# Performance work log

Hardware: AMD Instinct MI355X
Metric: run time of the kernel (lower is better)

The kernel has to match this reference:

```python
import jax, jax.numpy as jnp
import numpy as np
import math

DIM = 1024
D_FF = 1024
B = 128


def setup_inputs() -> dict:
    key = jax.random.key(0)
    ks = jax.random.split(key, 13)
    s = 1.0 / math.sqrt(DIM)
    sf = 1.0 / math.sqrt(D_FF)
    return {
        "x": jax.random.normal(ks[0], (B, DIM), dtype=jnp.float32),
        "Wq": jax.random.uniform(ks[1], (DIM, DIM), jnp.float32, -s, s),
        "bq": jax.random.uniform(ks[2], (DIM,), jnp.float32, -s, s),
        "Wk": jax.random.uniform(ks[3], (DIM, DIM), jnp.float32, -s, s),
        "bk": jax.random.uniform(ks[4], (DIM,), jnp.float32, -s, s),
        "Wv": jax.random.uniform(ks[5], (DIM, DIM), jnp.float32, -s, s),
        "bv": jax.random.uniform(ks[6], (DIM,), jnp.float32, -s, s),
        "Wo": jax.random.uniform(ks[7], (DIM, DIM), jnp.float32, -s, s),
        "bo": jax.random.uniform(ks[8], (DIM,), jnp.float32, -s, s),
        "W1": jax.random.uniform(ks[9], (D_FF, DIM), jnp.float32, -s, s),
        "b1": jax.random.uniform(ks[10], (D_FF,), jnp.float32, -s, s),
        "W2": jax.random.uniform(ks[11], (DIM, D_FF), jnp.float32, -sf, sf),
        "b2": jax.random.uniform(ks[12], (DIM,), jnp.float32, -sf, sf),
    }


def reference(x, Wq, bq, Wk, bk, Wv, bv, Wo, bo, W1, b1, W2, b2):
    # Attention (eval mode: dropout is identity)
    q = x @ Wq.T + bq                      # [B, D]
    k = x @ Wk.T + bk                      # [B, D]
    v = x @ Wv.T + bv                      # [B, D]
    inv_sqrt_dk = 1.0 / math.sqrt(DIM)
    # per-sample outer product: weights[b, i, j] = q[b,i] * k[b,j] / sqrt(d_k)
    weights = (q[:, :, None] * k[:, None, :]) * inv_sqrt_dk  # [B, D, D]
    nw = jax.nn.softmax(weights, axis=-1)                    # [B, D, D]
    attn_out = jnp.einsum('bij,bj->bi', nw, v)               # [B, D]
    attn_out = attn_out @ Wo.T + bo
    # residual 1
    x2 = x + attn_out
    # FFN
    h = jax.nn.relu(x2 @ W1.T + b1)        # [B, d_ff]
    ff = h @ W2.T + b2                     # [B, D]
    out = x2 + ff
    return (out, nw)
```

## Files before the change

kernel.cpp:

```cpp
#include <hip/hip_runtime.h>

#define DIM   1024
#define BATCH 128
#define MAT   (BATCH*DIM)
#define NROWS MAT
#define DS    32

typedef float f4n __attribute__((ext_vector_type(4)));

#define Q_AT  28672
#define A_WO  28672
#define B_WO  47104
#define A_W1  54272
#define B_W1  72704
#define A_W2  79872
#define B_W2  98304
#define MBASE 105472

struct Params {
  const float *x,*Wq,*bq,*Wk,*bk,*Wv,*bv,*Wo,*bo,*W1,*b1,*W2,*b2;
  float *out,*nw;
  float *q,*k,*v,*araw,*x2,*h,*P;
};

template<bool WRITE, bool AR>
__device__ __forceinline__ void attn_range(const Params& p, int r0, int r1, int lane)
{
  int bcur = -1;
  float4 kr[4], vr[4];
#pragma unroll 1
  for (int row = r0; row < r1; ++row) {
    const int b = row >> 10;
    if (b != bcur) {
      bcur = b;
      const float4* __restrict__ k4 = (const float4*)(p.k + ((size_t)b<<10));
#pragma unroll
      for (int t=0;t<4;++t) kr[t] = k4[lane + 64*t];
      if (AR) {
        const float4* __restrict__ v4 = (const float4*)(p.v + ((size_t)b<<10));
#pragma unroll
        for (int t=0;t<4;++t) vr[t] = v4[lane + 64*t];
      }
    }
    const float c = p.q[row] * 0.03125f;
    float sum=0.f, dot=0.f;
    float4 e[4];
#pragma unroll
    for (int t=0;t<4;++t) {
      const float4 kk = kr[t];
      float4 pp;
      pp.x=__expf(c*kk.x); pp.y=__expf(c*kk.y);
      pp.z=__expf(c*kk.z); pp.w=__expf(c*kk.w);
      sum += (pp.x+pp.y)+(pp.z+pp.w);
      if (AR) {
        const float4 vv = vr[t];
        dot += pp.x*vv.x + pp.y*vv.y + pp.z*vv.z + pp.w*vv.w;
      }
      e[t]=pp;
    }
#pragma unroll
    for (int off=32; off>=1; off>>=1) {
      sum += __shfl_xor(sum, off);
      if (AR) dot += __shfl_xor(dot, off);
    }
    const float rinv = 1.f/sum;
    if (WRITE) {
      f4n* o = (f4n*)(p.nw + ((size_t)row<<10));
#pragma unroll
      for (int t=0;t<4;++t) {
        const float4 pp=e[t];
        f4n st;
        st.x = pp.x*rinv; st.y = pp.y*rinv;
        st.z = pp.z*rinv; st.w = pp.w*rinv;
        __builtin_nontemporal_store(st, &o[lane + 64*t]);
      }
    }
    if (AR && lane==0) p.araw[row] = dot*rinv;
  }
}

__device__ __forceinline__ void gemm_tile(
    const float* __restrict__ X, const float* __restrict__ W,
    float* __restrict__ Pout, int n0, int k0, int KC,
    float* xt, float* wt)
{
  const int tid = threadIdx.x;
  const int tn = tid & 15, tb = tid >> 4;
  const int b_base = tb*8, n_base = tn*4;
  float acc[8][4];
#pragma unroll
  for (int i=0;i<8;++i)
#pragma unroll
    for (int j=0;j<4;++j) acc[i][j]=0.f;

  for (int s=0; s<KC/DS; ++s) {
    const int kk = k0 + s*DS;
#pragma unroll
    for (int r=0;r<4;++r) {
      const int row = (tid>>3) + 32*r;
      const int c0  = (tid&7)*4;
      const float4 vv = *(const float4*)(X + (size_t)row*DIM + kk + c0);
      xt[(c0+0)*132+row]=vv.x; xt[(c0+1)*132+row]=vv.y;
      xt[(c0+2)*132+row]=vv.z; xt[(c0+3)*132+row]=vv.w;
    }
#pragma unroll
    for (int r=0;r<2;++r) {
      const int row = (tid>>3) + 32*r;
      const int c0  = (tid&7)*4;
      const f4n vv = __builtin_nontemporal_load(
          (const f4n*)(W + (size_t)(n0+row)*DIM + kk + c0));
      wt[(c0+0)*68+row]=vv.x; wt[(c0+1)*68+row]=vv.y;
      wt[(c0+2)*68+row]=vv.z; wt[(c0+3)*68+row]=vv.w;
    }
    __syncthreads();
#pragma unroll 4
    for (int d=0; d<DS; ++d) {
      const float4 xa0 = *(const float4*)&xt[d*132 + b_base];
      const float4 xa1 = *(const float4*)&xt[d*132 + b_base + 4];
      const float4 wa  = *(const float4*)&wt[d*68  + n_base];
      const float xr[8] = {xa0.x,xa0.y,xa0.z,xa0.w, xa1.x,xa1.y,xa1.z,xa1.w};
      const float wr[4] = {wa.x,wa.y,wa.z,wa.w};
#pragma unroll
      for (int bb=0;bb<8;++bb)
#pragma unroll
        for (int nn=0;nn<4;++nn) acc[bb][nn] += xr[bb]*wr[nn];
    }
    __syncthreads();
  }
#pragma unroll
  for (int bb=0;bb<8;++bb) {
    const float4 st = make_float4(acc[bb][0],acc[bb][1],acc[bb][2],acc[bb][3]);
    *(float4*)(Pout + (size_t)(b_base+bb)*DIM + n0 + n_base) = st;
  }
}

__global__ __launch_bounds__(256) void qkv_partial(
    const float* __restrict__ X, const float* __restrict__ W0,
    const float* __restrict__ W1, const float* __restrict__ W2,
    float* __restrict__ P)
{
  __shared__ float xt[DS*132];
  __shared__ float wt[DS*68];
  const int z = blockIdx.z;
  const float* W = (z==0)?W0:(z==1)?W1:W2;
  gemm_tile(X, W, P + (size_t)(z*8+blockIdx.y)*MAT,
            blockIdx.x*64, blockIdx.y*128, 128, xt, wt);
}

__global__ __launch_bounds__(256) void qkv_reduce(Params p)
{
  const int t = blockIdx.x*256 + threadIdx.x;
  const int z = t >> 15, idx4 = t & 32767;
  const float4* Pz = (const float4*)(p.P + (size_t)z*8*MAT);
  const float*  bias = (z==0) ? p.bq : (z==1) ? p.bk : p.bv;
  float* outz = (z==0) ? p.q : (z==1) ? p.k : p.v;
  float4 s = Pz[idx4];
#pragma unroll
  for (int sp=1; sp<8; ++sp) {
    const float4 t2 = Pz[sp*(MAT/4)+idx4];
    s.x+=t2.x; s.y+=t2.y; s.z+=t2.z; s.w+=t2.w;
  }
  const float4 b4 = ((const float4*)bias)[idx4 & 255];
  s.x+=b4.x; s.y+=b4.y; s.z+=b4.z; s.w+=b4.w;
  ((float4*)outz)[idx4] = s;
}

__global__ __launch_bounds__(256,4) void attn_mixed(Params p)
{
  const int bid = blockIdx.x, tid = threadIdx.x;
  const int wave = tid>>6, lane = tid&63;
  if (bid < 768) {
    const int gw = bid*4 + wave;
    int r0 = gw*43, r1 = r0 + 43;
    if (r1 > NROWS) r1 = NROWS;
    attn_range<false,true>(p, r0, r1, lane);
  } else {
    const int gw2 = (bid-768)*4 + wave;
    attn_range<true,false>(p, gw2*28, gw2*28 + 28, lane);
  }
}

__global__ __launch_bounds__(256,4) void chainA(Params p,
    const float* __restrict__ X, const float* __restrict__ W, int wbase)
{
  __shared__ float xt[DS*132];
  __shared__ float wt[DS*68];
  const int bid = blockIdx.x, tid = threadIdx.x;
  const int wave = tid>>6, lane = tid&63;
  if (bid < 256) {
    gemm_tile(X, W, p.P + (size_t)(bid&15)*MAT, (bid>>4)*64, (bid&15)*64, 64, xt, wt);
  } else {
    const int gw = (bid-256)*4 + wave;
    attn_range<true,false>(p, wbase + gw*6, wbase + gw*6 + 6, lane);
  }
}

__global__ __launch_bounds__(256,4) void chainB(Params p,
    const float* __restrict__ bias, const float* __restrict__ extra,
    float* __restrict__ out, int relu, int wbase)
{
  const int bid = blockIdx.x, tid = threadIdx.x;
  const int wave = tid>>6, lane = tid&63;
  if (bid < 128) {
    const int idx4 = bid*256 + tid;
    const float4* P4 = (const float4*)p.P;
    float4 s = P4[idx4];
#pragma unroll
    for (int sp=1; sp<16; ++sp) {
      const float4 t2 = P4[sp*(MAT/4)+idx4];
      s.x+=t2.x; s.y+=t2.y; s.z+=t2.z; s.w+=t2.w;
    }
    const float4 b4 = ((const float4*)bias)[idx4 & 255];
    s.x+=b4.x; s.y+=b4.y; s.z+=b4.z; s.w+=b4.w;
    if (relu) { s.x=fmaxf(s.x,0.f); s.y=fmaxf(s.y,0.f);
                s.z=fmaxf(s.z,0.f); s.w=fmaxf(s.w,0.f); }
    if (extra) {
      const float4 e = ((const float4*)extra)[idx4];
      s.x+=e.x; s.y+=e.y; s.z+=e.z; s.w+=e.w;
    }
    ((float4*)out)[idx4] = s;
  } else {
    const int gw = (bid-128)*4 + wave;
    attn_range<true,false>(p, wbase + gw*2, wbase + gw*2 + 2, lane);
  }
}

__global__ __launch_bounds__(256,4) void mopup(Params p)
{
  const int gw = blockIdx.x*4 + (threadIdx.x>>6);
  const int lane = threadIdx.x & 63;
  int r0, n;
  if (gw < 1024) { r0 = MBASE + gw*7;             n = 7; }
  else           { r0 = MBASE + 7168 + (gw-1024)*6; n = 6; }
  attn_range<true,false>(p, r0, r0 + n, lane);
}

extern "C" void kernel_launch(void* const* d_in, const int* in_sizes, int n_in,
                              void* d_out, int out_size, void* d_ws, size_t ws_size,
                              hipStream_t stream)
{
  (void)in_sizes; (void)n_in; (void)out_size; (void)ws_size;
  Params p;
  p.x  = (const float*)d_in[0];
  p.Wq = (const float*)d_in[1];  p.bq = (const float*)d_in[2];
  p.Wk = (const float*)d_in[3];  p.bk = (const float*)d_in[4];
  p.Wv = (const float*)d_in[5];  p.bv = (const float*)d_in[6];
  p.Wo = (const float*)d_in[7];  p.bo = (const float*)d_in[8];
  p.W1 = (const float*)d_in[9];  p.b1 = (const float*)d_in[10];
  p.W2 = (const float*)d_in[11]; p.b2 = (const float*)d_in[12];
  p.out = (float*)d_out;
  p.nw  = p.out + MAT;
  float* ws = (float*)d_ws;
  p.q    = ws;         p.k  = ws + MAT;   p.v = ws + 2*MAT;
  p.araw = ws + 3*MAT; p.x2 = ws + 4*MAT; p.h = ws + 5*MAT;
  p.P    = ws + 6*MAT;

  qkv_partial<<<dim3(16,8,3), 256, 0, stream>>>(p.x, p.Wq, p.Wk, p.Wv, p.P);
  qkv_reduce<<<384, 256, 0, stream>>>(p);

  attn_mixed<<<1024, 256, 0, stream>>>(p);

  chainA<<<1024, 256, 0, stream>>>(p, p.araw, p.Wo, A_WO);
  chainB<<<1024, 256, 0, stream>>>(p, p.bo, p.x, p.x2, 0, B_WO);

  chainA<<<1024, 256, 0, stream>>>(p, p.x2, p.W1, A_W1);
  chainB<<<1024, 256, 0, stream>>>(p, p.b1, nullptr, p.h, 1, B_W1);

  chainA<<<1024, 256, 0, stream>>>(p, p.h, p.W2, A_W2);
  chainB<<<1024, 256, 0, stream>>>(p, p.b2, p.x2, p.out, 0, B_W2);

  mopup<<<1024, 256, 0, stream>>>(p);
}
```

Baseline: 177.7 us.

## Cache softmax reciprocal sums and deepen split-K in chained GEMM stages

The first attention pass, which already computes each row's softmax sum for the attention output, now also saves the reciprocal sum to a workspace buffer. Every later pass that writes normalized weights reuses it, so those passes do only exp, scale and store, with no cross-lane sum reduction. The chained Wo/W1/W2 GEMMs move from 16-way to 32-way split-K with 512 GEMM blocks. The row ranges given to each overlapped stage are rebalanced to match. In exchange the workspace needs room for one more buffer plus twice as many partial-sum slabs, and each reduce step reads 32 partials instead of 16.

```diff
diff --git a/kernel.cpp b/kernel.cpp
--- a/kernel.cpp
+++ b/kernel.cpp
@@ -10,21 +10,21 @@
 
 #define Q_AT  28672
 #define A_WO  28672
-#define B_WO  47104
-#define A_W1  54272
-#define B_W1  72704
-#define A_W2  79872
-#define B_W2  98304
-#define MBASE 105472
+#define B_WO  43008
+#define A_W1  50176
+#define B_W1  64512
+#define A_W2  71680
+#define B_W2  86016
+#define MBASE 93184
 
 struct Params {
   const float *x,*Wq,*bq,*Wk,*bk,*Wv,*bv,*Wo,*bo,*W1,*b1,*W2,*b2;
   float *out,*nw;
-  float *q,*k,*v,*araw,*x2,*h,*P;
+  float *q,*k,*v,*araw,*x2,*h,*rinv,*P;
 };
 
-template<bool WRITE, bool AR>
-__device__ __forceinline__ void attn_range(const Params& p, int r0, int r1, int lane)
+template<bool WRITE, bool AR, bool USE_RINV>
+__device__ __forceinline__ void attn_rows(const Params& p, int r0, int r1, int lane)
 {
   int bcur = -1;
   float4 kr[4], vr[4];
@@ -43,6 +43,21 @@
       }
     }
     const float c = p.q[row] * 0.03125f;
+
+    if (WRITE && USE_RINV) {
+      const float rinv = p.rinv[row];
+      f4n* o = (f4n*)(p.nw + ((size_t)row<<10));
+#pragma unroll
+      for (int t=0;t<4;++t) {
+        const float4 kk = kr[t];
+        f4n st;
+        st.x = __expf(c*kk.x)*rinv; st.y = __expf(c*kk.y)*rinv;
+        st.z = __expf(c*kk.z)*rinv; st.w = __expf(c*kk.w)*rinv;
+        __builtin_nontemporal_store(st, &o[lane + 64*t]);
+      }
+      continue;
+    }
+
     float sum=0.f, dot=0.f;
     float4 e[4];
 #pragma unroll
@@ -75,7 +90,7 @@
         __builtin_nontemporal_store(st, &o[lane + 64*t]);
       }
     }
-    if (AR && lane==0) p.araw[row] = dot*rinv;
+    if (AR && lane==0) { p.araw[row] = dot*rinv; p.rinv[row] = rinv; }
   }
 }
 
@@ -173,10 +188,10 @@
     const int gw = bid*4 + wave;
     int r0 = gw*43, r1 = r0 + 43;
     if (r1 > NROWS) r1 = NROWS;
-    attn_range<false,true>(p, r0, r1, lane);
+    attn_rows<false,true,false>(p, r0, r1, lane);
   } else {
     const int gw2 = (bid-768)*4 + wave;
-    attn_range<true,false>(p, gw2*28, gw2*28 + 28, lane);
+    attn_rows<true,false,false>(p, gw2*28, gw2*28 + 28, lane);
   }
 }
 
@@ -187,11 +202,12 @@
   __shared__ float wt[DS*68];
   const int bid = blockIdx.x, tid = threadIdx.x;
   const int wave = tid>>6, lane = tid&63;
-  if (bid < 256) {
-    gemm_tile(X, W, p.P + (size_t)(bid&15)*MAT, (bid>>4)*64, (bid&15)*64, 64, xt, wt);
+  if (bid < 512) {
+    const int nt = bid >> 5, sp = bid & 31;
+    gemm_tile(X, W, p.P + (size_t)sp*MAT, nt*64, sp*32, 32, xt, wt);
   } else {
-    const int gw = (bid-256)*4 + wave;
-    attn_range<true,false>(p, wbase + gw*6, wbase + gw*6 + 6, lane);
+    const int gw = (bid-512)*4 + wave;
+    attn_rows<true,false,true>(p, wbase + gw*7, wbase + gw*7 + 7, lane);
   }
 }
 
@@ -206,7 +222,7 @@
     const float4* P4 = (const float4*)p.P;
     float4 s = P4[idx4];
 #pragma unroll
-    for (int sp=1; sp<16; ++sp) {
+    for (int sp=1; sp<32; ++sp) {
       const float4 t2 = P4[sp*(MAT/4)+idx4];
       s.x+=t2.x; s.y+=t2.y; s.z+=t2.z; s.w+=t2.w;
     }
@@ -221,7 +237,7 @@
     ((float4*)out)[idx4] = s;
   } else {
     const int gw = (bid-128)*4 + wave;
-    attn_range<true,false>(p, wbase + gw*2, wbase + gw*2 + 2, lane);
+    attn_rows<true,false,true>(p, wbase + gw*2, wbase + gw*2 + 2, lane);
   }
 }
 
@@ -230,9 +246,9 @@
   const int gw = blockIdx.x*4 + (threadIdx.x>>6);
   const int lane = threadIdx.x & 63;
   int r0, n;
-  if (gw < 1024) { r0 = MBASE + gw*7;             n = 7; }
-  else           { r0 = MBASE + 7168 + (gw-1024)*6; n = 6; }
-  attn_range<true,false>(p, r0, r0 + n, lane);
+  if (gw < 1024) { r0 = MBASE + gw*10;               n = 10; }
+  else           { r0 = MBASE + 10240 + (gw-1024)*9; n = 9;  }
+  attn_rows<true,false,true>(p, r0, r0 + n, lane);
 }
 
 extern "C" void kernel_launch(void* const* d_in, const int* in_sizes, int n_in,
@@ -251,9 +267,9 @@
   p.out = (float*)d_out;
   p.nw  = p.out + MAT;
   float* ws = (float*)d_ws;
-  p.q    = ws;         p.k  = ws + MAT;   p.v = ws + 2*MAT;
-  p.araw = ws + 3*MAT; p.x2 = ws + 4*MAT; p.h = ws + 5*MAT;
-  p.P    = ws + 6*MAT;
+  p.q    = ws;         p.k    = ws + MAT;   p.v = ws + 2*MAT;
+  p.araw = ws + 3*MAT; p.x2   = ws + 4*MAT; p.h = ws + 5*MAT;
+  p.rinv = ws + 6*MAT; p.P    = ws + 7*MAT;
 
   qkv_partial<<<dim3(16,8,3), 256, 0, stream>>>(p.x, p.Wq, p.Wk, p.Wv, p.P);
   qkv_reduce<<<384, 256, 0, stream>>>(p);
```

After: 186.8 us. 1.05x slower.
